# Optimization experiments

Hardware: AMD Instinct MI355X
Metric: run time of the kernel (lower is better)

## Reference

```python
import jax, jax.numpy as jnp
import numpy as np

WS = 4        # window_size
SHIFT = 2     # shift
NHEADS = 8


def setup_inputs():
    key = jax.random.key(0)
    k = jax.random.split(key, 5)
    N, C, H, W = 16, 512, 96, 96
    x = jax.random.normal(k[0], (N, C, H, W), dtype=jnp.float32)
    # nn.MultiheadAttention parameters
    in_proj_w = jax.random.normal(k[1], (3 * C, C), dtype=jnp.float32) * 0.02
    in_proj_b = jax.random.normal(k[2], (3 * C,), dtype=jnp.float32) * 0.02
    out_w = jax.random.normal(k[3], (C, C), dtype=jnp.float32) * 0.02
    out_b = jax.random.normal(k[4], (C,), dtype=jnp.float32) * 0.02
    return {"x": x, "in_proj_w": in_proj_w, "in_proj_b": in_proj_b,
            "out_w": out_w, "out_b": out_b}


def _split_window(x, ws):
    # replicates torch: cat(split(x, ws, dim=3), dim=2); cat(split(x, ws, dim=2), dim=0)
    N, C, Hp, Wp = x.shape
    nh, nw = Hp // ws, Wp // ws
    x = x.reshape(N, C, nh, ws, nw, ws)      # n c ib wi jb wj
    x = x.transpose(4, 2, 0, 1, 3, 5)        # jb ib n c wi wj (col-block outermost in batch)
    return x.reshape(nw * nh * N, C, ws, ws), nh, nw


def _concat_window(x, nh, nw, ws):
    # inverse of _split_window, replicating torch chunk/cat order
    N = x.shape[0] // (nh * nw)
    C = x.shape[1]
    x = x.reshape(nw, nh, N, C, ws, ws)      # jb ib n c wi wj
    x = x.transpose(2, 3, 1, 4, 0, 5)        # n c ib wi jb wj
    return x.reshape(N, C, nh * ws, nw * ws)


def _mha(xt, mask_f, in_proj_w, in_proj_b, out_w, out_b):
    # xt: (B, L, C); mask_f: (B, L) FLOAT key_padding_mask -> added to logits (torch semantics)
    B, L, C = xt.shape
    d = C // NHEADS
    qkv = xt @ in_proj_w.T + in_proj_b                     # (B, L, 3C)
    q, k, v = jnp.split(qkv, 3, axis=-1)
    heads = lambda t: t.reshape(B, L, NHEADS, d).transpose(0, 2, 1, 3)  # (B, H, L, d)
    q, k, v = heads(q), heads(k), heads(v)
    scale = float(1.0 / np.sqrt(d))
    scores = jnp.einsum('bhqd,bhkd->bhqk', q, k) * scale
    scores = scores + mask_f[:, None, None, :]             # additive float key mask
    attn = jax.nn.softmax(scores, axis=-1)
    o = jnp.einsum('bhqk,bhkd->bhqd', attn, v)
    o = o.transpose(0, 2, 1, 3).reshape(B, L, C)
    return o @ out_w.T + out_b


def reference(x, in_proj_w, in_proj_b, out_w, out_b):
    N, C, H, W = x.shape
    ws = WS
    pad_h, pad_w = ws - H % ws, ws - W % ws   # note: pads a full window even when divisible
    x = jnp.pad(x, ((0, 0), (0, 0), (0, pad_h), (0, pad_w)))
    x = jnp.roll(x, (SHIFT, SHIFT), axis=(2, 3))
    # BUG-FAITHFUL: source overwrites the boolean mask with a second roll of x,
    # so the "mask" is the doubly-rolled float feature map.
    mask = jnp.roll(x, (SHIFT, SHIFT), axis=(2, 3))
    xw, nh, nw = _split_window(x, ws)
    mw, _, _ = _split_window(mask, ws)
    B = xw.shape[0]
    xt = xw.reshape(B, C, ws * ws).transpose(0, 2, 1)      # (B, L=ws*ws, C)
    mask_f = mw[:, 0].reshape(B, ws * ws)                  # channel-0 float "mask"
    ot = _mha(xt, mask_f, in_proj_w, in_proj_b, out_w, out_b)
    ow = ot.transpose(0, 2, 1).reshape(B, C, ws, ws)
    out = _concat_window(ow, nh, nw, ws)
    out = jnp.roll(out, (-SHIFT, -SHIFT), axis=(2, 3))
    return out[:, :, :H, :W]
```

## Files before the change

kernel.cpp:

```cpp
#include <hip/hip_runtime.h>
#include <cstdint>


typedef __attribute__((ext_vector_type(8))) __bf16 bf16x8;
typedef __attribute__((ext_vector_type(8))) uint16_t u16x8;
typedef __attribute__((ext_vector_type(4))) float f32x4;

__device__ __forceinline__ uint16_t f2bf(float f) {
  union { float f; uint32_t u; } c; c.f = f;
  uint32_t r = c.u + 0x7FFFu + ((c.u >> 16) & 1u);
  return (uint16_t)(r >> 16);
}
__device__ __forceinline__ float bf2f(uint16_t u) {
  union { uint32_t u; float f; } c; c.u = ((uint32_t)u) << 16;
  return c.f;
}

__device__ __forceinline__ void g2lds16(const void* g, void* lds) {
  __builtin_amdgcn_global_load_lds(
      (const __attribute__((address_space(1))) uint32_t*)(uintptr_t)g,
      (__attribute__((address_space(3))) uint32_t*)(uintptr_t)lds,
      16, 0, 0);
}

#define CFENCE asm volatile("" ::: "memory")
#define BAR do { CFENCE; __builtin_amdgcn_s_barrier(); CFENCE; } while (0)
#define SCHED0 __builtin_amdgcn_sched_barrier(0)

__global__ void cvt_weights(const float* __restrict__ w1, const float* __restrict__ w2,
                            uint16_t* __restrict__ o1, uint16_t* __restrict__ o2) {
  int i = blockIdx.x * 256 + threadIdx.x;
  if (i < 786432) o1[i] = f2bf(w1[i]);
  if (i < 262144) o2[i] = f2bf(w2[i]);
}

__global__ __launch_bounds__(256) void gather_kernel(
    const float* __restrict__ x, uint16_t* __restrict__ xbf, int n0) {
  __shared__ float tile[64][65];
  const int z = blockIdx.z;
  const int g = z / 100, hh = z % 100;
  const int c0 = blockIdx.y * 64, ww0 = blockIdx.x * 64;
  const int n = n0 + g;
  const int hp = (hh >= 2) ? hh - 2 : hh + 98;
  const bool hok = hp < 96;
  const int t = threadIdx.x;
  const int lane = t & 63, grp = t >> 6;

  const int ww = ww0 + lane;
  const int wp = (ww >= 2) ? ww - 2 : ww + 98;
  const bool wok = hok && (ww < 100) && (wp < 96);
  const float* xb = x + ((size_t)n * 512) * 9216 + (size_t)hp * 96 + wp;
#pragma unroll
  for (int i = 0; i < 16; ++i) {
    int c = grp + i * 4;
    tile[c][lane] = wok ? xb[(size_t)(c0 + c) * 9216] : 0.f;
  }
  __syncthreads();
#pragma unroll
  for (int i = 0; i < 16; ++i) {
    int wl = grp + i * 4;
    int www = ww0 + wl;
    if (www < 100) {
      int m = (g * 625 + (hh >> 2) * 25 + (www >> 2)) * 16 + (hh & 3) * 4 + (www & 3);
      xbf[(size_t)m * 512 + c0 + lane] = f2bf(tile[lane][wl]);
    }
  }
}

template <int EPI, int NB, int MODE>
__global__ __launch_bounds__(512, 2) void gemm8(
    const uint16_t* __restrict__ A, const uint16_t* __restrict__ B,
    const float* __restrict__ bias, uint16_t* __restrict__ Cbf,
    float* __restrict__ Cout, int Mg, int n0) {
  __shared__ alignas(16) uint16_t lds[65536];
  const int t = threadIdx.x;
  const int w = t >> 6, lane = t & 63;
  const int wr = w >> 2, wc = w & 3;
  const int lr = lane & 15, lg = lane >> 4;

  const int nwg = gridDim.x, bid = blockIdx.x;
  const int q = nwg >> 3, r = nwg & 7;
  const int xc = bid & 7, li = bid >> 3;
  const int wg = (xc < r ? xc * (q + 1) : r * (q + 1) + (xc - r) * q) + li;
  int bm, bn;
  if (MODE == 0) { bm = wg / NB; bn = wg % NB; }
  else           { bm = wg % NB; bn = wg / NB; }

  auto STAGE = [&](int kt, int h) {
    const uint16_t* src = (h < 2) ? A : B;
    const int row0 = ((h < 2) ? bm * 256 : bn * 256) + (h & 1) * 128;
    const int base = ((h < 2) ? 0 : 32768) + (kt & 1) * 16384 + (h & 1) * 8192;
#pragma unroll
    for (int i = 0; i < 2; ++i) {
      int e = i * 512 + t;
      int row = e >> 3, slot = e & 7;
      const uint16_t* gp = src + (size_t)(row0 + row) * 512 + kt * 64 +
                           ((slot ^ (row & 7)) << 3);
      g2lds16(gp, &lds[base + ((i * 512 + w * 64) << 3)]);
    }
  };
  auto LDA = [&](int cur, int mi, int k2) -> bf16x8 {
    int row = wr * 128 + mi * 16 + lr;
    int byte = cur * 32768 + row * 128 + (((k2 * 32 + lg * 8) * 2) ^ ((row & 7) << 4));
    return *(const bf16x8*)((const char*)lds + byte);
  };
  auto LDB = [&](int cur, int ni, int k2) -> bf16x8 {
    int row = wc * 64 + ni * 16 + lr;
    int byte = 65536 + cur * 32768 + row * 128 +
               (((k2 * 32 + lg * 8) * 2) ^ ((row & 7) << 4));
    return *(const bf16x8*)((const char*)lds + byte);
  };
  auto MM = [&](bf16x8 av, bf16x8 bv, f32x4 c) -> f32x4 {
    if constexpr (EPI == 0) return __builtin_amdgcn_mfma_f32_16x16x32_bf16(bv, av, c, 0, 0, 0);
    else                    return __builtin_amdgcn_mfma_f32_16x16x32_bf16(av, bv, c, 0, 0, 0);
  };

  f32x4 acc[8][4];
#pragma unroll
  for (int mi = 0; mi < 8; ++mi)
#pragma unroll
    for (int ni = 0; ni < 4; ++ni) acc[mi][ni] = (f32x4){0.f, 0.f, 0.f, 0.f};

  STAGE(0, 0); STAGE(0, 1); STAGE(0, 2); STAGE(0, 3);
  STAGE(1, 0); STAGE(1, 1);
  asm volatile("s_waitcnt vmcnt(4)" ::: "memory");
  BAR;

#define MQUAD(AF, BF, MIOFF, NIOFF)                                         \
  __builtin_amdgcn_s_setprio(1);                                            \
  _Pragma("unroll") for (int mi = 0; mi < 4; ++mi)                          \
  _Pragma("unroll") for (int ni = 0; ni < 2; ++ni)                          \
  _Pragma("unroll") for (int k2 = 0; k2 < 2; ++k2)                          \
      acc[mi + MIOFF][ni + NIOFF] =                                         \
          MM(AF[mi][k2], BF[ni][k2], acc[mi + MIOFF][ni + NIOFF]);          \
  __builtin_amdgcn_s_setprio(0);

  for (int j = 0; j < 8; ++j) {
    const int cur = j & 1;
    bf16x8 a0[4][2], a1[4][2], b0[2][2], b1[2][2];
#pragma unroll
    for (int mi = 0; mi < 4; ++mi)
#pragma unroll
      for (int k2 = 0; k2 < 2; ++k2) a0[mi][k2] = LDA(cur, mi, k2);
#pragma unroll
    for (int ni = 0; ni < 2; ++ni)
#pragma unroll
      for (int k2 = 0; k2 < 2; ++k2) b0[ni][k2] = LDB(cur, ni, k2);
    if (j + 1 < 8) STAGE(j + 1, 2);
    BAR; SCHED0;
    MQUAD(a0, b0, 0, 0);
    BAR;
#pragma unroll
    for (int mi = 0; mi < 4; ++mi)
#pragma unroll
      for (int k2 = 0; k2 < 2; ++k2) a1[mi][k2] = LDA(cur, mi + 4, k2);
#pragma unroll
    for (int ni = 0; ni < 2; ++ni)
#pragma unroll
      for (int k2 = 0; k2 < 2; ++k2) b1[ni][k2] = LDB(cur, ni + 2, k2);
    if (j + 1 < 8) STAGE(j + 1, 3);
    BAR; SCHED0;
    MQUAD(a1, b1, 4, 2);
    BAR;
    if (j + 2 < 8) STAGE(j + 2, 0);
    BAR; SCHED0;
    MQUAD(a0, b1, 0, 2);
    BAR;
    if (j + 2 < 8) STAGE(j + 2, 1);
    if (j < 6) { asm volatile("s_waitcnt vmcnt(4)" ::: "memory"); }
    else       { asm volatile("s_waitcnt vmcnt(0)" ::: "memory"); }
    BAR; SCHED0;
    MQUAD(a1, b0, 4, 0);
    BAR;
  }
#undef MQUAD

  __syncthreads();

  if (EPI == 0) {
    uint16_t* ldsE = lds;
#pragma unroll
    for (int p = 0; p < 2; ++p) {
      if (wr == p) {
#pragma unroll
        for (int mi = 0; mi < 8; ++mi)
#pragma unroll
          for (int ni = 0; ni < 4; ++ni) {
            const float* b4 = &bias[bn * 256 + wc * 64 + ni * 16 + lg * 4];
            uint16_t pk[4];
#pragma unroll
            for (int rr = 0; rr < 4; ++rr) pk[rr] = f2bf(acc[mi][ni][rr] + b4[rr]);
            uint2 v; v.x = (uint32_t)pk[0] | ((uint32_t)pk[1] << 16);
            v.y = (uint32_t)pk[2] | ((uint32_t)pk[3] << 16);
            *(uint2*)&ldsE[(mi * 16 + lr) * 272 + wc * 64 + ni * 16 + lg * 4] = v;
          }
      }
      __syncthreads();
#pragma unroll
      for (int i = 0; i < 8; ++i) {
        int e = i * 512 + t;
        int mrow = e >> 5, ch = e & 31;
        int m = bm * 256 + p * 128 + mrow;
        *(uint4*)&Cbf[(size_t)m * 1536 + bn * 256 + ch * 8] =
            *(const uint4*)&ldsE[mrow * 272 + ch * 8];
      }
      __syncthreads();
    }
  } else {
    float* ldsF = (float*)lds;
    const int Gwin = Mg >> 4;
#pragma unroll
    for (int p = 0; p < 4; ++p) {
      if (wc == p) {
#pragma unroll
        for (int mi = 0; mi < 8; ++mi) {
          const float* b4 = &bias[bm * 256 + wr * 128 + mi * 16 + lg * 4];
#pragma unroll
          for (int ni = 0; ni < 4; ++ni)
#pragma unroll
            for (int rr = 0; rr < 4; ++rr)
              ldsF[(wr * 128 + mi * 16 + lg * 4 + rr) * 68 + ni * 16 + lr] =
                  acc[mi][ni][rr] + b4[rr];
        }
      }
      __syncthreads();
#pragma unroll
      for (int i = 0; i < 8; ++i) {
        int e = i * 512 + t;
        int w4 = e & 3, rrow = (e >> 2) & 3, c = e >> 4;
        int cw = bn * 16 + p * 4 + w4;
        if (cw < Gwin) {
          int g = cw / 625, wid = cw % 625;
          int ib = wid / 25, jb = wid % 25;
          int hh = ib * 4 + rrow;
          if (hh >= 2 && hh < 98) {
            float4 v = *(const float4*)&ldsF[c * 68 + w4 * 16 + rrow * 4];
            size_t base = ((size_t)(n0 + g) * 512 + bm * 256 + c) * 9216 +
                          (size_t)(hh - 2) * 96;
            if (jb >= 1 && jb < 24) {
              float* pp = &Cout[base + jb * 4 - 2];
              float2 lo; lo.x = v.x; lo.y = v.y;
              float2 hi; hi.x = v.z; hi.y = v.w;
              *(float2*)pp = lo;
              *(float2*)(pp + 2) = hi;
            } else if (jb == 0) {
              Cout[base + 0] = v.z; Cout[base + 1] = v.w;
            } else {
              Cout[base + 94] = v.x; Cout[base + 95] = v.y;
            }
          }
        }
      }
      __syncthreads();
    }
  }
}

__global__ __launch_bounds__(128) void attn_kernel(
    const uint16_t* __restrict__ qkv, const float* __restrict__ x,
    uint16_t* __restrict__ obuf, int n0) {
  __shared__ alignas(16) uint16_t skv[16][1024];
  __shared__ float smask[16];
  const int b = blockIdx.x;
  const int g = b / 625, wid = b % 625;
  const int ib = wid / 25, jb = wid % 25;
  const int t = threadIdx.x;
  const int wv = t >> 6;
  const int mbase = b * 16;
  const int h = t >> 4, qi = t & 15;

#pragma unroll
  for (int it = 0; it < 16; ++it) {
    int e = it * 128 + t;
    int l = e >> 7, c = e & 127;
    const uint16_t* src = qkv + (size_t)(mbase + l) * 1536 + 512 + c * 8;
    g2lds16(src, (uint16_t*)skv + (it * 128 + wv * 64) * 8);
  }
  float qv[64];
#pragma unroll
  for (int d8 = 0; d8 < 8; ++d8) {
    u16x8 v = *(const u16x8*)&qkv[(size_t)(mbase + qi) * 1536 + h * 64 + d8 * 8];
#pragma unroll
    for (int j = 0; j < 8; ++j) qv[d8 * 8 + j] = bf2f(v[j]);
  }
  if (t < 16) {
    int hh = ib * 4 + (t >> 2), ww = jb * 4 + (t & 3);
    int a = (hh >= 4) ? hh - 4 : hh + 96;
    int c = (ww >= 4) ? ww - 4 : ww + 96;
    smask[t] = (a < 96 && c < 96)
                   ? x[((size_t)(n0 + g) * 512) * 9216 + (size_t)a * 96 + c]
                   : 0.f;
  }
  __syncthreads();

  float s[16];
  float mx = -1e30f;
#pragma unroll
  for (int ki = 0; ki < 16; ++ki) {
    float a = 0.f;
#pragma unroll
    for (int d8 = 0; d8 < 8; ++d8) {
      u16x8 kv = *(const u16x8*)&skv[ki][h * 64 + d8 * 8];
#pragma unroll
      for (int j = 0; j < 8; ++j) a += qv[d8 * 8 + j] * bf2f(kv[j]);
    }
    s[ki] = a * 0.125f + smask[ki];
    mx = fmaxf(mx, s[ki]);
  }
  float sum = 0.f;
#pragma unroll
  for (int ki = 0; ki < 16; ++ki) { s[ki] = __expf(s[ki] - mx); sum += s[ki]; }
  const float inv = 1.f / sum;
  float o[64];
#pragma unroll
  for (int d = 0; d < 64; ++d) o[d] = 0.f;
#pragma unroll
  for (int ki = 0; ki < 16; ++ki) {
    float wgt = s[ki] * inv;
#pragma unroll
    for (int d8 = 0; d8 < 8; ++d8) {
      u16x8 vv = *(const u16x8*)&skv[ki][512 + h * 64 + d8 * 8];
#pragma unroll
      for (int j = 0; j < 8; ++j) o[d8 * 8 + j] += wgt * bf2f(vv[j]);
    }
  }
  const int m = mbase + qi;
#pragma unroll
  for (int d8 = 0; d8 < 8; ++d8) {
    alignas(16) uint16_t tmp[8];
#pragma unroll
    for (int j = 0; j < 8; ++j) tmp[j] = f2bf(o[d8 * 8 + j]);
    *(uint4*)&obuf[(size_t)m * 512 + h * 64 + d8 * 8] = *(uint4*)tmp;
  }
}

extern "C" void kernel_launch(void* const* d_in, const int* in_sizes, int n_in,
                              void* d_out, int out_size, void* d_ws, size_t ws_size,
                              hipStream_t stream) {
  const float* x  = (const float*)d_in[0];
  const float* wq = (const float*)d_in[1];
  const float* bq = (const float*)d_in[2];
  const float* wo = (const float*)d_in[3];
  const float* bo = (const float*)d_in[4];
  float* out = (float*)d_out;
  uint8_t* ws = (uint8_t*)d_ws;

  uint16_t* wq_bf = (uint16_t*)ws;
  uint16_t* wo_bf = (uint16_t*)(ws + 1572864);
  uint8_t* bufbase = ws + 2097152;

  int G = 16;
  while (G > 1) {
    int Mg = G * 10000;
    int Mp = ((Mg + 255) / 256) * 256;
    size_t need = (size_t)2097152 + (size_t)Mp * 4096;
    if (need <= ws_size) break;
    G >>= 1;
  }
  const int Mg = G * 10000;
  const int Mp = ((Mg + 255) / 256) * 256;
  uint16_t* xo   = (uint16_t*)bufbase;
  uint16_t* qkvb = (uint16_t*)(bufbase + (size_t)Mp * 1024);

  cvt_weights<<<dim3(3072), dim3(256), 0, stream>>>(wq, wo, wq_bf, wo_bf);

  for (int n0 = 0; n0 < 16; n0 += G) {
    gather_kernel<<<dim3(2, 8, G * 100), dim3(256), 0, stream>>>(x, xo, n0);
    gemm8<0, 6, 0><<<dim3((Mp / 256) * 6), dim3(512), 0, stream>>>(
        xo, wq_bf, bq, qkvb, nullptr, Mg, n0);
    attn_kernel<<<dim3(G * 625), dim3(128), 0, stream>>>(qkvb, x, xo, n0);
    gemm8<1, 2, 1><<<dim3((Mp / 256) * 2), dim3(512), 0, stream>>>(
        wo_bf, xo, bo, nullptr, out, Mg, n0);
  }
  (void)in_sizes; (void)n_in; (void)out_size;
}
```

Baseline: 1.139 ms.

## Replace quad-phase pipelined GEMM with simple double-buffered loop and direct epilogue

The finely interleaved GEMM main loop is replaced by a plain two-buffer loop. Previously it staged A and B halves at different phases and split the MFMAs into four quadrants with barriers between them. Now each step loads the next full K-tile of A and B into the alternate buffer, then issues all 64 MFMAs per wave, then waits for the loads and syncs once. The QKV epilogue drops the LDS-transposed 16-byte stores and writes bf16 values straight to global memory one element at a time. This removes barriers and scheduling constraints, but it risks less overlap between loads and compute, higher register pressure from holding all fragments, and poorly coalesced output stores.

```diff
diff --git a/kernel.cpp b/kernel.cpp
--- a/kernel.cpp
+++ b/kernel.cpp
@@ -25,7 +25,6 @@
 
 #define CFENCE asm volatile("" ::: "memory")
 #define BAR do { CFENCE; __builtin_amdgcn_s_barrier(); CFENCE; } while (0)
-#define SCHED0 __builtin_amdgcn_sched_barrier(0)
 
 __global__ void cvt_weights(const float* __restrict__ w1, const float* __restrict__ w2,
                             uint16_t* __restrict__ o1, uint16_t* __restrict__ o2) {
@@ -68,7 +67,7 @@
 }
 
 template <int EPI, int NB, int MODE>
-__global__ __launch_bounds__(512, 2) void gemm8(
+__global__ __launch_bounds__(512, 2) void gemm2(
     const uint16_t* __restrict__ A, const uint16_t* __restrict__ B,
     const float* __restrict__ bias, uint16_t* __restrict__ Cbf,
     float* __restrict__ Cout, int Mg, int n0) {
@@ -86,34 +85,30 @@
   if (MODE == 0) { bm = wg / NB; bn = wg % NB; }
   else           { bm = wg % NB; bn = wg / NB; }
 
-  auto STAGE = [&](int kt, int h) {
-    const uint16_t* src = (h < 2) ? A : B;
-    const int row0 = ((h < 2) ? bm * 256 : bn * 256) + (h & 1) * 128;
-    const int base = ((h < 2) ? 0 : 32768) + (kt & 1) * 16384 + (h & 1) * 8192;
-#pragma unroll
-    for (int i = 0; i < 2; ++i) {
+  auto STAGE = [&](int kt, int b) {
+#pragma unroll
+    for (int i = 0; i < 4; ++i) {
       int e = i * 512 + t;
       int row = e >> 3, slot = e & 7;
-      const uint16_t* gp = src + (size_t)(row0 + row) * 512 + kt * 64 +
+      const uint16_t* ga = A + (size_t)(bm * 256 + row) * 512 + kt * 64 +
                            ((slot ^ (row & 7)) << 3);
-      g2lds16(gp, &lds[base + ((i * 512 + w * 64) << 3)]);
+      const uint16_t* gb = B + (size_t)(bn * 256 + row) * 512 + kt * 64 +
+                           ((slot ^ (row & 7)) << 3);
+      g2lds16(ga, &lds[b * 32768 + ((i * 512 + w * 64) << 3)]);
+      g2lds16(gb, &lds[b * 32768 + 16384 + ((i * 512 + w * 64) << 3)]);
     }
   };
-  auto LDA = [&](int cur, int mi, int k2) -> bf16x8 {
+  auto LDA = [&](int b, int mi, int k2) -> bf16x8 {
     int row = wr * 128 + mi * 16 + lr;
-    int byte = cur * 32768 + row * 128 + (((k2 * 32 + lg * 8) * 2) ^ ((row & 7) << 4));
+    int byte = b * 65536 + row * 128 + ((k2 * 64 + lg * 16) ^ ((row & 7) << 4));
     return *(const bf16x8*)((const char*)lds + byte);
   };
-  auto LDB = [&](int cur, int ni, int k2) -> bf16x8 {
+  auto LDB = [&](int b, int ni, int k2) -> bf16x8 {
     int row = wc * 64 + ni * 16 + lr;
-    int byte = 65536 + cur * 32768 + row * 128 +
-               (((k2 * 32 + lg * 8) * 2) ^ ((row & 7) << 4));
+    int byte = b * 65536 + 32768 + row * 128 +
+               ((k2 * 64 + lg * 16) ^ ((row & 7) << 4));
     return *(const bf16x8*)((const char*)lds + byte);
   };
-  auto MM = [&](bf16x8 av, bf16x8 bv, f32x4 c) -> f32x4 {
-    if constexpr (EPI == 0) return __builtin_amdgcn_mfma_f32_16x16x32_bf16(bv, av, c, 0, 0, 0);
-    else                    return __builtin_amdgcn_mfma_f32_16x16x32_bf16(av, bv, c, 0, 0, 0);
-  };
 
   f32x4 acc[8][4];
 #pragma unroll
@@ -121,92 +116,52 @@
 #pragma unroll
     for (int ni = 0; ni < 4; ++ni) acc[mi][ni] = (f32x4){0.f, 0.f, 0.f, 0.f};
 
-  STAGE(0, 0); STAGE(0, 1); STAGE(0, 2); STAGE(0, 3);
-  STAGE(1, 0); STAGE(1, 1);
-  asm volatile("s_waitcnt vmcnt(4)" ::: "memory");
+  STAGE(0, 0);
+  asm volatile("s_waitcnt vmcnt(0)" ::: "memory");
   BAR;
 
-#define MQUAD(AF, BF, MIOFF, NIOFF)                                         \
-  __builtin_amdgcn_s_setprio(1);                                            \
-  _Pragma("unroll") for (int mi = 0; mi < 4; ++mi)                          \
-  _Pragma("unroll") for (int ni = 0; ni < 2; ++ni)                          \
-  _Pragma("unroll") for (int k2 = 0; k2 < 2; ++k2)                          \
-      acc[mi + MIOFF][ni + NIOFF] =                                         \
-          MM(AF[mi][k2], BF[ni][k2], acc[mi + MIOFF][ni + NIOFF]);          \
-  __builtin_amdgcn_s_setprio(0);
-
-  for (int j = 0; j < 8; ++j) {
-    const int cur = j & 1;
-    bf16x8 a0[4][2], a1[4][2], b0[2][2], b1[2][2];
-#pragma unroll
-    for (int mi = 0; mi < 4; ++mi)
-#pragma unroll
-      for (int k2 = 0; k2 < 2; ++k2) a0[mi][k2] = LDA(cur, mi, k2);
-#pragma unroll
-    for (int ni = 0; ni < 2; ++ni)
-#pragma unroll
-      for (int k2 = 0; k2 < 2; ++k2) b0[ni][k2] = LDB(cur, ni, k2);
-    if (j + 1 < 8) STAGE(j + 1, 2);
-    BAR; SCHED0;
-    MQUAD(a0, b0, 0, 0);
+  int cur = 0;
+  for (int k = 0; k < 8; ++k) {
+    if (k + 1 < 8) STAGE(k + 1, cur ^ 1);
+    bf16x8 af[8][2], bf[4][2];
+#pragma unroll
+    for (int mi = 0; mi < 8; ++mi)
+#pragma unroll
+      for (int k2 = 0; k2 < 2; ++k2) af[mi][k2] = LDA(cur, mi, k2);
+#pragma unroll
+    for (int ni = 0; ni < 4; ++ni)
+#pragma unroll
+      for (int k2 = 0; k2 < 2; ++k2) bf[ni][k2] = LDB(cur, ni, k2);
+    __builtin_amdgcn_s_setprio(1);
+#pragma unroll
+    for (int mi = 0; mi < 8; ++mi)
+#pragma unroll
+      for (int ni = 0; ni < 4; ++ni)
+#pragma unroll
+        for (int k2 = 0; k2 < 2; ++k2)
+          acc[mi][ni] = __builtin_amdgcn_mfma_f32_16x16x32_bf16(
+              af[mi][k2], bf[ni][k2], acc[mi][ni], 0, 0, 0);
+    __builtin_amdgcn_s_setprio(0);
+    asm volatile("s_waitcnt vmcnt(0)" ::: "memory");
     BAR;
-#pragma unroll
-    for (int mi = 0; mi < 4; ++mi)
-#pragma unroll
-      for (int k2 = 0; k2 < 2; ++k2) a1[mi][k2] = LDA(cur, mi + 4, k2);
-#pragma unroll
-    for (int ni = 0; ni < 2; ++ni)
-#pragma unroll
-      for (int k2 = 0; k2 < 2; ++k2) b1[ni][k2] = LDB(cur, ni + 2, k2);
-    if (j + 1 < 8) STAGE(j + 1, 3);
-    BAR; SCHED0;
-    MQUAD(a1, b1, 4, 2);
-    BAR;
-    if (j + 2 < 8) STAGE(j + 2, 0);
-    BAR; SCHED0;
-    MQUAD(a0, b1, 0, 2);
-    BAR;
-    if (j + 2 < 8) STAGE(j + 2, 1);
-    if (j < 6) { asm volatile("s_waitcnt vmcnt(4)" ::: "memory"); }
-    else       { asm volatile("s_waitcnt vmcnt(0)" ::: "memory"); }
-    BAR; SCHED0;
-    MQUAD(a1, b0, 4, 0);
-    BAR;
-  }
-#undef MQUAD
-
-  __syncthreads();
+    cur ^= 1;
+  }
 
   if (EPI == 0) {
-    uint16_t* ldsE = lds;
-#pragma unroll
-    for (int p = 0; p < 2; ++p) {
-      if (wr == p) {
-#pragma unroll
-        for (int mi = 0; mi < 8; ++mi)
-#pragma unroll
-          for (int ni = 0; ni < 4; ++ni) {
-            const float* b4 = &bias[bn * 256 + wc * 64 + ni * 16 + lg * 4];
-            uint16_t pk[4];
-#pragma unroll
-            for (int rr = 0; rr < 4; ++rr) pk[rr] = f2bf(acc[mi][ni][rr] + b4[rr]);
-            uint2 v; v.x = (uint32_t)pk[0] | ((uint32_t)pk[1] << 16);
-            v.y = (uint32_t)pk[2] | ((uint32_t)pk[3] << 16);
-            *(uint2*)&ldsE[(mi * 16 + lr) * 272 + wc * 64 + ni * 16 + lg * 4] = v;
-          }
+#pragma unroll
+    for (int ni = 0; ni < 4; ++ni) {
+      int col = bn * 256 + wc * 64 + ni * 16 + lr;
+      float bb = bias[col];
+#pragma unroll
+      for (int mi = 0; mi < 8; ++mi) {
+        int row = bm * 256 + wr * 128 + mi * 16 + lg * 4;
+#pragma unroll
+        for (int rr = 0; rr < 4; ++rr)
+          Cbf[(size_t)(row + rr) * 1536 + col] = f2bf(acc[mi][ni][rr] + bb);
       }
-      __syncthreads();
-#pragma unroll
-      for (int i = 0; i < 8; ++i) {
-        int e = i * 512 + t;
-        int mrow = e >> 5, ch = e & 31;
-        int m = bm * 256 + p * 128 + mrow;
-        *(uint4*)&Cbf[(size_t)m * 1536 + bn * 256 + ch * 8] =
-            *(const uint4*)&ldsE[mrow * 272 + ch * 8];
-      }
-      __syncthreads();
     }
   } else {
+    __syncthreads();
     float* ldsF = (float*)lds;
     const int Gwin = Mg >> 4;
 #pragma unroll
@@ -366,10 +321,10 @@
 
   for (int n0 = 0; n0 < 16; n0 += G) {
     gather_kernel<<<dim3(2, 8, G * 100), dim3(256), 0, stream>>>(x, xo, n0);
-    gemm8<0, 6, 0><<<dim3((Mp / 256) * 6), dim3(512), 0, stream>>>(
+    gemm2<0, 6, 0><<<dim3((Mp / 256) * 6), dim3(512), 0, stream>>>(
         xo, wq_bf, bq, qkvb, nullptr, Mg, n0);
     attn_kernel<<<dim3(G * 625), dim3(128), 0, stream>>>(qkvb, x, xo, n0);
-    gemm8<1, 2, 1><<<dim3((Mp / 256) * 2), dim3(512), 0, stream>>>(
+    gemm2<1, 2, 1><<<dim3((Mp / 256) * 2), dim3(512), 0, stream>>>(
         wo_bf, xo, bo, nullptr, out, Mg, n0);
   }
   (void)in_sizes; (void)n_in; (void)out_size;
```

Measured after the change: 1.172 ms. 2.9% more time.
